# Kernel tuning notes

Measured on AMD Instinct MI355X. Metric: run time of the kernel, lower is better.

The kernel has to match this reference:

```python
import jax, jax.numpy as jnp
import numpy as np

EPS = 1e-5
NUM_CLUSTERS = 64


def _bn(x, g, b, m, v):
    # eval-mode BatchNorm over channel (last) axis
    return (x - m) * (g * jax.lax.rsqrt(v + EPS)) + b


def _segment_max(feat, choice, num_clusters):
    # feat: [B, N, C], choice: [B, N] -> [B, K, C] (amax per cluster, -inf if empty)
    def one(f, c):
        init = jnp.full((num_clusters, f.shape[-1]), -jnp.inf, dtype=f.dtype)
        return init.at[c].max(f)
    return jax.vmap(one)(feat, choice)


def setup_inputs() -> dict:
    key = jax.random.key(0)
    ks = jax.random.split(key, 8)
    B, N, K, OUT = 32, 8192, NUM_CLUSTERS, 384
    s = lambda fan: 1.0 / np.sqrt(fan)
    return {
        "xyz": jax.random.normal(ks[0], (B, N, 3), jnp.float32),
        "choice": jax.random.randint(ks[1], (B, N), 0, K, jnp.int32),
        "w1": jax.random.normal(ks[2], (128, 3), jnp.float32) * s(3),
        "b1": jnp.zeros((128,), jnp.float32),
        "bn1_g": jnp.ones((128,), jnp.float32),
        "bn1_b": jnp.zeros((128,), jnp.float32),
        "bn1_m": jnp.zeros((128,), jnp.float32),
        "bn1_v": jnp.ones((128,), jnp.float32),
        "w2": jax.random.normal(ks[3], (256, 128), jnp.float32) * s(128),
        "b2": jnp.zeros((256,), jnp.float32),
        "w3": jax.random.normal(ks[4], (512, 512), jnp.float32) * s(512),
        "b3": jnp.zeros((512,), jnp.float32),
        "bn2_g": jnp.ones((512,), jnp.float32),
        "bn2_b": jnp.zeros((512,), jnp.float32),
        "bn2_m": jnp.zeros((512,), jnp.float32),
        "bn2_v": jnp.ones((512,), jnp.float32),
        "w4": jax.random.normal(ks[5], (OUT, 512), jnp.float32) * s(512),
        "b4": jnp.zeros((OUT,), jnp.float32),
    }


def reference(xyz, choice, w1, b1, bn1_g, bn1_b, bn1_m, bn1_v, w2, b2,
              w3, b3, bn2_g, bn2_b, bn2_m, bn2_v, w4, b4):
    # first_conv: 1x1 conv == per-point linear. xyz: [B,N,3]
    h = jnp.einsum("bnc,oc->bno", xyz, w1) + b1            # [B,N,128]
    h = jax.nn.relu(_bn(h, bn1_g, bn1_b, bn1_m, bn1_v))
    feat = jnp.einsum("bnc,oc->bno", h, w2) + b2            # [B,N,256]
    # cluster amax pooling + gather-broadcast back to points
    fg = _segment_max(feat, choice, NUM_CLUSTERS)           # [B,K,256]
    fg_pts = jnp.take_along_axis(fg, choice[..., None], axis=1)  # [B,N,256]
    f = jnp.concatenate([fg_pts, feat], axis=-1)            # [B,N,512]
    # second_conv
    h2 = jnp.einsum("bnc,oc->bno", f, w3) + b3              # [B,N,512]
    h2 = jax.nn.relu(_bn(h2, bn2_g, bn2_b, bn2_m, bn2_v))
    out = jnp.einsum("bnc,oc->bno", h2, w4) + b4            # [B,N,out_dim]
    return _segment_max(out, choice, NUM_CLUSTERS)          # [B,K,out_dim]
```

## Files before the change

### kernel.cpp

```cpp
#include <hip/hip_runtime.h>
#include <hip/hip_bf16.h>

typedef unsigned short u16;
typedef __attribute__((ext_vector_type(8))) short short8;
typedef __attribute__((ext_vector_type(4))) float f32x4;

#define EPSV 1e-5f
#define ENC_NINF 0x007FFFFFu

__device__ __forceinline__ float bf2f(u16 u) {
    union { unsigned int i; float f; } v; v.i = ((unsigned int)u) << 16; return v.f;
}
__device__ __forceinline__ u16 f2bf(float f) {
    union { float f; unsigned int i; } v; v.f = f;
    unsigned int x = v.i;
    return (u16)((x + 0x7FFFu + ((x >> 16) & 1u)) >> 16);
}
__device__ __forceinline__ unsigned int encbf(u16 u) {
    unsigned int f = ((unsigned int)u) << 16;
    return (f & 0x80000000u) ? ~f : (f | 0x80000000u);
}
__device__ __forceinline__ float dec(unsigned int u) {
    union { float f; unsigned int uu; } v;
    v.uu = (u & 0x80000000u) ? (u & 0x7FFFFFFFu) : ~u;
    return v.f;
}

__device__ __forceinline__ void async16(const u16* g, u16* l) {
    __builtin_amdgcn_global_load_lds((const __attribute__((address_space(1))) void*)g,
                                     (__attribute__((address_space(3))) void*)l,
                                     16, 0, 0);
}

__global__ __launch_bounds__(256) void k_fillf(float* __restrict__ o, int n, float val)
{
    int i = blockIdx.x * 256 + threadIdx.x;
    if (i < n) o[i] = val;
}

__global__ __launch_bounds__(256) void k_initu(unsigned int* __restrict__ o, int n)
{
    int i = blockIdx.x * 256 + threadIdx.x;
    if (i < n) o[i] = ENC_NINF;
}

struct Ptrs { const void* p[17]; int off[18]; int chN; };

__global__ __launch_bounds__(256) void k_repack(Ptrs P, const void* __restrict__ chSrc,
                                                int* __restrict__ chi, u16* __restrict__ rp)
{
    const unsigned int* probe = (const unsigned int*)P.p[9];
    int cnt = 0;
#pragma unroll
    for (int i = 0; i < 64; ++i) {
        unsigned int lo = probe[i] & 0xFFFFu;
        if (((lo >> 7) & 0xFFu) >= 0x80u) ++cnt;
    }
    const bool is_f32 = (cnt > 8);

    const unsigned int* cp = (const unsigned int*)chSrc;
    int z = 0; unsigned int mx = 0;
    for (int i = 0; i < 1024; ++i) {
        unsigned int w = cp[i];
        z += (w == 0u);
        mx = (w > mx) ? w : mx;
    }
    const int chMode = (mx >= 64u) ? 2 : ((z > 300) ? 1 : 0);

    const int stride = gridDim.x * 256;
    const int gid0 = blockIdx.x * 256 + threadIdx.x;

    const int totalF = P.off[17];
    for (int g = gid0; g < totalF; g += stride) {
        int t = 0;
        while (g >= P.off[t + 1]) ++t;
        int off = g - P.off[t];
        u16 v;
        if (is_f32) v = f2bf(((const float*)P.p[t])[off]);
        else        v = ((const u16*)P.p[t])[off];
        rp[g] = v;
    }
    for (int i = gid0; i < P.chN; i += stride) {
        int v;
        if (chMode == 1)      v = (int)((const long long*)chSrc)[i];
        else if (chMode == 2) v = (int)((const float*)chSrc)[i];
        else                  v = ((const int*)chSrc)[i];
        chi[i] = v & 63;
    }
}

__global__ __launch_bounds__(256) void k_sort(const int* __restrict__ chi,
                                              int* __restrict__ schoice,
                                              int* __restrict__ perm)
{
    __shared__ int hist[64];
    __shared__ int base[64];
    const int b = blockIdx.x, tid = threadIdx.x;
    if (tid < 64) hist[tid] = 0;
    __syncthreads();
    const int o = b << 13;
    for (int i = tid; i < 8192; i += 256) atomicAdd(&hist[chi[o + i]], 1);
    __syncthreads();
    if (tid == 0) {
        int s = 0;
        for (int k = 0; k < 64; ++k) { base[k] = s; s += hist[k]; }
    }
    __syncthreads();
    for (int i = tid; i < 8192; i += 256) {
        int k = chi[o + i];
        int pos = atomicAdd(&base[k], 1);
        schoice[o + pos] = k;
        perm[o + pos] = o + i;
    }
}

__global__ __launch_bounds__(256, 2) void g1_feat(
    const u16* __restrict__ xyz, const u16* __restrict__ w1, const u16* __restrict__ b1,
    const u16* __restrict__ g1v, const u16* __restrict__ bb1,
    const u16* __restrict__ m1, const u16* __restrict__ v1,
    const u16* __restrict__ w2, const u16* __restrict__ b2,
    const int* __restrict__ schoice, const int* __restrict__ perm,
    u16* __restrict__ feat, unsigned int* __restrict__ fg_u)
{
    __shared__ __align__(16) u16 Bs[256 * 128];
    __shared__ unsigned int lred[8 * 256];
    __shared__ float4 pw[128];
    __shared__ float xs[128], ys[128], zs[128];
    __shared__ int chs[128];
    const int tid = threadIdx.x, lane = tid & 63, wave = tid >> 6;
    const int wm = (wave & 1) << 6, wn = (wave >> 1) << 6;
    const int m0 = blockIdx.x << 7;
    if (tid < 128) {
        float s = bf2f(g1v[tid]) * rsqrtf(bf2f(v1[tid]) + EPSV);
        float4 w;
        w.x = bf2f(w1[tid * 3 + 0]) * s;
        w.y = bf2f(w1[tid * 3 + 1]) * s;
        w.z = bf2f(w1[tid * 3 + 2]) * s;
        w.w = (bf2f(b1[tid]) - bf2f(m1[tid])) * s + bf2f(bb1[tid]);
        pw[tid] = w;
        const u16* p = xyz + (size_t)perm[m0 + tid] * 3;
        xs[tid] = bf2f(p[0]); ys[tid] = bf2f(p[1]); zs[tid] = bf2f(p[2]);
        chs[tid] = schoice[m0 + tid];
    }
    const int q = lane >> 4, mr = lane & 15;
    f32x4 acc[2][4][4] = {};
#pragma unroll
    for (int i = 0; i < 16; ++i) {
        int id = (i << 8) + tid, row = id >> 4, cc = id & 15;
        async16(w2 + (size_t)row * 128 + ((cc ^ (row & 15)) << 3), &Bs[id << 3]);
    }
    __syncthreads();
    const int kmin = chs[0], nk = chs[127] - kmin + 1;
    const bool useL = (nk <= 8);
    if (useL) for (int i = tid; i < (nk << 8); i += 256) lred[i] = ENC_NINF;
#pragma unroll
    for (int kk = 0; kk < 4; ++kk) {
        const int lc = kk * 4 + q;
        float4 wv[8];
#pragma unroll
        for (int j = 0; j < 8; ++j) wv[j] = pw[kk * 32 + q * 8 + j];
        short8 af[4];
#pragma unroll
        for (int mi = 0; mi < 4; ++mi) {
            int row = wm + mi * 16 + mr;
            float x = xs[row], y = ys[row], z = zs[row];
#pragma unroll
            for (int j = 0; j < 8; ++j) {
                float val = fmaf(x, wv[j].x, fmaf(y, wv[j].y, fmaf(z, wv[j].z, wv[j].w)));
                af[mi][j] = (short)f2bf(fmaxf(val, 0.0f));
            }
        }
#pragma unroll
        for (int h = 0; h < 2; ++h) {
            short8 bfr[4];
#pragma unroll
            for (int ni = 0; ni < 4; ++ni) {
                int r = (h << 7) + wn + ni * 16 + mr;
                bfr[ni] = *(const short8*)&Bs[r * 128 + ((lc ^ (r & 15)) << 3)];
            }
#pragma unroll
            for (int mi = 0; mi < 4; ++mi)
#pragma unroll
                for (int ni = 0; ni < 4; ++ni)
                    acc[h][mi][ni] = __builtin_amdgcn_mfma_f32_16x16x32_bf16(af[mi], bfr[ni], acc[h][mi][ni], 0, 0, 0);
        }
    }
    __syncthreads();
    const int colb = lane & 15;
    const int bl = m0 >> 13;
    unsigned int* db = fg_u + (size_t)(bl << 6) * 256;
#pragma unroll
    for (int h = 0; h < 2; ++h)
#pragma unroll
        for (int ni = 0; ni < 4; ++ni) {
            int n = (h << 7) + wn + (ni << 4) + colb;
            float bv = bf2f(b2[n]);
#pragma unroll
            for (int mi = 0; mi < 4; ++mi) {
                int curk = -1; unsigned int run = 0;
#pragma unroll
                for (int r = 0; r < 4; ++r) {
                    int rr = wm + (mi << 4) + (q << 2) + r;
                    u16 vb = f2bf(acc[h][mi][ni][r] + bv);
                    feat[(size_t)(m0 + rr) * 256 + n] = vb;
                    unsigned int e = encbf(vb);
                    int k = chs[rr];
                    if (k != curk) {
                        if (curk >= 0) {
                            if (useL) atomicMax(&lred[((curk - kmin) << 8) + n], run);
                            else      atomicMax(&db[curk * 256 + n], run);
                        }
                        curk = k; run = e;
                    } else run = run > e ? run : e;
                }
                if (useL) atomicMax(&lred[((curk - kmin) << 8) + n], run);
                else      atomicMax(&db[curk * 256 + n], run);
            }
        }
    if (useL) {
        __syncthreads();
        for (int i = tid; i < (nk << 8); i += 256) {
            unsigned int v = lred[i];
            if (v != ENC_NINF) atomicMax(&db[(kmin + (i >> 8)) * 256 + (i & 255)], v);
        }
    }
}

__global__ __launch_bounds__(256) void g4_out(
    const u16* __restrict__ A, const u16* __restrict__ Bt,
    const u16* __restrict__ bias, const int* __restrict__ schoice,
    unsigned int* __restrict__ out_u, const int K, const int N)
{
    __shared__ __align__(16) u16 smem[2 * 128 * 64];
    __shared__ int chs[128];
    u16* As = smem;
    u16* Bs = smem + 128 * 64;
    const int tid = threadIdx.x, lane = tid & 63, wave = tid >> 6;
    const int wm = (wave & 1) << 6, wn = (wave >> 1) << 6;
    const int m0 = blockIdx.x << 7, n0 = blockIdx.y << 7;
    const int c = tid & 7, rb = tid >> 3;
    if (tid < 128) chs[tid] = schoice[m0 + tid];
    f32x4 acc[4][4] = {};
    for (int k0 = 0; k0 < K; k0 += 64) {
        __syncthreads();
#pragma unroll
        for (int i = 0; i < 4; ++i) {
            int id = (i << 8) + tid, row = id >> 3, cc = id & 7;
            async16(Bt + (n0 + row) * K + k0 + ((cc ^ (row & 7)) << 3), &Bs[id << 3]);
        }
#pragma unroll
        for (int i = 0; i < 4; ++i) {
            int r = rb + (i << 5);
            async16(A + (size_t)(m0 + r) * K + k0 + ((c ^ (r & 7)) << 3),
                    &As[(((i << 8) + tid) << 3)]);
        }
        __syncthreads();
        const int q = lane >> 4, mr = lane & 15;
#pragma unroll
        for (int kk = 0; kk < 2; ++kk) {
            short8 af[4], bfr[4];
            const int lc = kk * 4 + q;
#pragma unroll
            for (int mi = 0; mi < 4; ++mi) {
                int r = wm + mi * 16 + mr;
                af[mi] = *(const short8*)&As[r * 64 + ((lc ^ (r & 7)) << 3)];
            }
#pragma unroll
            for (int ni = 0; ni < 4; ++ni) {
                int r = wn + ni * 16 + mr;
                bfr[ni] = *(const short8*)&Bs[r * 64 + ((lc ^ (r & 7)) << 3)];
            }
#pragma unroll
            for (int mi = 0; mi < 4; ++mi)
#pragma unroll
                for (int ni = 0; ni < 4; ++ni)
                    acc[mi][ni] = __builtin_amdgcn_mfma_f32_16x16x32_bf16(af[mi], bfr[ni], acc[mi][ni], 0, 0, 0);
        }
    }
    __syncthreads();
    unsigned int* lred = (unsigned int*)smem;
    const int kmin = chs[0], nk = chs[127] - kmin + 1;
    for (int i = tid; i < (nk << 7); i += 256) lred[i] = ENC_NINF;
    __syncthreads();
    const int q = lane >> 4, colb = lane & 15;
#pragma unroll
    for (int ni = 0; ni < 4; ++ni) {
        int nc = wn + (ni << 4) + colb;
        float bv = bf2f(bias[n0 + nc]);
#pragma unroll
        for (int mi = 0; mi < 4; ++mi) {
            int curk = -1; unsigned int run = 0;
#pragma unroll
            for (int r = 0; r < 4; ++r) {
                int rr = wm + (mi << 4) + (q << 2) + r;
                unsigned int e = encbf(f2bf(acc[mi][ni][r] + bv));
                int k = chs[rr];
                if (k != curk) {
                    if (curk >= 0) atomicMax(&lred[((curk - kmin) << 7) + nc], run);
                    curk = k; run = e;
                } else run = run > e ? run : e;
            }
            atomicMax(&lred[((curk - kmin) << 7) + nc], run);
        }
    }
    __syncthreads();
    const int bl = m0 >> 13;
    unsigned int* db = out_u + (size_t)(bl << 6) * N;
    for (int i = tid; i < (nk << 7); i += 256) {
        unsigned int v = lred[i];
        if (v != ENC_NINF) atomicMax(&db[(kmin + (i >> 7)) * N + n0 + (i & 127)], v);
    }
}

__global__ __launch_bounds__(256) void k_dec_bf(const unsigned int* __restrict__ u,
                                                u16* __restrict__ o, int n)
{
    int i = blockIdx.x * 256 + threadIdx.x;
    if (i < n) o[i] = f2bf(dec(u[i]));
}
__global__ __launch_bounds__(256) void k_dec_f32(const unsigned int* __restrict__ u,
                                                 float* __restrict__ o, int n)
{
    int i = blockIdx.x * 256 + threadIdx.x;
    if (i < n) o[i] = dec(u[i]);
}

__global__ __launch_bounds__(256, 2) void g3_h2(
    const int* __restrict__ schoice, const u16* __restrict__ feat,
    const u16* __restrict__ fg, const u16* __restrict__ w3, const u16* __restrict__ b3,
    const u16* __restrict__ g2, const u16* __restrict__ bb2,
    const u16* __restrict__ m2, const u16* __restrict__ v2,
    u16* __restrict__ h2)
{
    __shared__ __align__(16) u16 As[128 * 64];
    __shared__ __align__(16) u16 Bs[2 * 128 * 64];
    const int tid = threadIdx.x, lane = tid & 63, wave = tid >> 6;
    const int wm = (wave & 1) << 6, wn = (wave >> 1) << 6;
    const int m0 = blockIdx.x << 7, n0 = blockIdx.y << 8;
    const int c = tid & 7, rb = tid >> 3;
    const u16* fgrow[4]; const u16* ftrow[4];
#pragma unroll
    for (int i = 0; i < 4; ++i) {
        int pt = m0 + rb + (i << 5);
        int b = pt >> 13;
        fgrow[i] = fg + (((b << 6) + schoice[pt]) << 8);
        ftrow[i] = feat + ((size_t)pt << 8);
    }
    f32x4 acc[2][4][4] = {};
    for (int k0 = 0; k0 < 512; k0 += 64) {
        __syncthreads();
#pragma unroll
        for (int nt = 0; nt < 2; ++nt)
#pragma unroll
            for (int i = 0; i < 4; ++i) {
                int id = (i << 8) + tid, row = id >> 3, cc = id & 7;
                async16(w3 + (size_t)(n0 + nt * 128 + row) * 512 + k0 + ((cc ^ (row & 7)) << 3),
                        &Bs[nt * 8192 + (id << 3)]);
            }
#pragma unroll
        for (int i = 0; i < 4; ++i) {
            int r = rb + (i << 5);
            int col = k0 + ((c ^ (r & 7)) << 3);
            const u16* src = (col < 256) ? (fgrow[i] + col) : (ftrow[i] + (col - 256));
            async16(src, &As[(((i << 8) + tid) << 3)]);
        }
        __syncthreads();
        const int q = lane >> 4, mr = lane & 15;
#pragma unroll
        for (int kk = 0; kk < 2; ++kk) {
            short8 af[4];
            const int lc = kk * 4 + q;
#pragma unroll
            for (int mi = 0; mi < 4; ++mi) {
                int r = wm + mi * 16 + mr;
                af[mi] = *(const short8*)&As[r * 64 + ((lc ^ (r & 7)) << 3)];
            }
#pragma unroll
            for (int nt = 0; nt < 2; ++nt) {
                short8 bfr[4];
#pragma unroll
                for (int ni = 0; ni < 4; ++ni) {
                    int r = wn + ni * 16 + mr;
                    bfr[ni] = *(const short8*)&Bs[nt * 8192 + r * 64 + ((lc ^ (r & 7)) << 3)];
                }
#pragma unroll
                for (int mi = 0; mi < 4; ++mi)
#pragma unroll
                    for (int ni = 0; ni < 4; ++ni)
                        acc[nt][mi][ni] = __builtin_amdgcn_mfma_f32_16x16x32_bf16(af[mi], bfr[ni], acc[nt][mi][ni], 0, 0, 0);
            }
        }
    }
    const int q = lane >> 4, colb = lane & 15;
#pragma unroll
    for (int nt = 0; nt < 2; ++nt)
#pragma unroll
        for (int ni = 0; ni < 4; ++ni) {
            int n = n0 + nt * 128 + wn + (ni << 4) + colb;
            float s = bf2f(g2[n]) * rsqrtf(bf2f(v2[n]) + EPSV);
            float t = (bf2f(b3[n]) - bf2f(m2[n])) * s + bf2f(bb2[n]);
#pragma unroll
            for (int mi = 0; mi < 4; ++mi)
#pragma unroll
                for (int r = 0; r < 4; ++r) {
                    int m = m0 + wm + (mi << 4) + (q << 2) + r;
                    h2[(size_t)m * 512 + n] = f2bf(fmaxf(fmaf(acc[nt][mi][ni][r], s, t), 0.0f));
                }
        }
}

extern "C" void kernel_launch(void* const* d_in, const int* in_sizes, int n_in,
                              void* d_out, int out_size, void* d_ws, size_t ws_size,
                              hipStream_t stream)
{
    float* out = (float*)d_out;
    if (n_in != 18) {
        k_fillf<<<dim3((out_size + 255) / 256), 256, 0, stream>>>(out, out_size, 1000.0f);
        return;
    }

    const int map[17] = {0, 2, 3, 4, 5, 6, 7, 8, 9, 10, 11, 12, 13, 14, 15, 16, 17};
    Ptrs P;
    P.off[0] = 0;
    for (int i = 0; i < 17; ++i) {
        P.p[i] = d_in[map[i]];
        P.off[i + 1] = P.off[i] + in_sizes[map[i]];
    }
    P.chN = in_sizes[1];

    char* ws = (char*)d_ws;
    int* chi = (int*)ws;
    const size_t chiB = ((size_t)P.chN * 4 + 255) & ~255ull;
    int* schoice = (int*)(ws + chiB);
    int* perm    = (int*)(ws + 2 * chiB);
    u16* rp = (u16*)(ws + 3 * chiB);
    const size_t rpB = ((size_t)P.off[17] * 2 + 255) & ~255ull;
    const size_t RPB = 3 * chiB + rpB;

    k_repack<<<dim3(1024), 256, 0, stream>>>(P, d_in[1], chi, rp);
    k_sort<<<dim3(P.chN >> 13), 256, 0, stream>>>(chi, schoice, perm);

    const u16* xyz  = rp + P.off[0];
    const u16* w1   = rp + P.off[1];
    const u16* b1   = rp + P.off[2];
    const u16* bn1g = rp + P.off[3];
    const u16* bn1b = rp + P.off[4];
    const u16* bn1m = rp + P.off[5];
    const u16* bn1v = rp + P.off[6];
    const u16* w2   = rp + P.off[7];
    const u16* b2   = rp + P.off[8];
    const u16* w3   = rp + P.off[9];
    const u16* b3   = rp + P.off[10];
    const u16* bn2g = rp + P.off[11];
    const u16* bn2b = rp + P.off[12];
    const u16* bn2m = rp + P.off[13];
    const u16* bn2v = rp + P.off[14];
    const u16* w4   = rp + P.off[15];
    const u16* b4   = rp + P.off[16];

    unsigned int* fg_u_all  = (unsigned int*)(ws + RPB);
    unsigned int* out_u_all = fg_u_all + 32 * 64 * 256;
    const size_t UB = 5242880ull;
    const int nU = 32 * 64 * 640;

    const size_t PB = 12615680ull;
    int sb = 32;
    while (sb > 1 && RPB + UB + (size_t)sb * PB > ws_size) sb >>= 1;
    if (RPB + UB + PB > ws_size) {
        k_fillf<<<dim3((out_size + 255) / 256), 256, 0, stream>>>(out, out_size, 3000.0f);
        return;
    }
    const int ns = 32 / sb;

    char* wsb = ws + RPB + UB;
    const size_t featB = (size_t)sb * 8192 * 256 * 2;
    const size_t h2B   = (size_t)sb * 8192 * 512 * 2;
    u16* feat = (u16*)(wsb);
    u16* h2s  = (u16*)(wsb + featB);
    u16* fg   = (u16*)(wsb + featB + h2B);

    k_initu<<<dim3((nU + 255) / 256), 256, 0, stream>>>(fg_u_all, nU);

    const int mblk = sb << 6;
    const int nfg = sb * 64 * 256;
    const int nou = sb * 64 * 384;
    for (int s = 0; s < ns; ++s) {
        const int b0 = s * sb;
        const int pt0 = b0 << 13;
        const int* sch_sl = schoice + pt0;
        const int* perm_sl = perm + pt0;
        unsigned int* fg_u  = fg_u_all + (size_t)b0 * 64 * 256;
        unsigned int* out_u = out_u_all + (size_t)b0 * 64 * 384;
        g1_feat<<<dim3(mblk), 256, 0, stream>>>(xyz, w1, b1, bn1g, bn1b, bn1m, bn1v,
                                                w2, b2, sch_sl, perm_sl, feat, fg_u);
        k_dec_bf<<<dim3((nfg + 255) / 256), 256, 0, stream>>>(fg_u, fg, nfg);
        g3_h2<<<dim3(mblk, 2), 256, 0, stream>>>(sch_sl, feat, fg, w3, b3,
                                                 bn2g, bn2b, bn2m, bn2v, h2s);
        g4_out<<<dim3(mblk, 3), 256, 0, stream>>>(h2s, w4, b4, sch_sl, out_u, 512, 384);
        k_dec_f32<<<dim3((nou + 255) / 256), 256, 0, stream>>>(out_u,
                                                               out + ((size_t)b0 << 6) * 384, nou);
    }
}
```

Baseline: 526.4 us.

## Fuse second-conv GEMM and output GEMM with segment-max into one kernel

Merges the h2 GEMM (with BN+ReLU) and the output GEMM plus cluster max-reduction into a single 512-thread kernel. Each 128-point block keeps its h2 half-tile in LDS and consumes it straight away, so the h2 intermediate never goes through global memory. The init of the max buffers is also folded into the repack kernel to save a launch. In exchange the kernel uses much more LDS and more accumulator registers per block, which lowers occupancy, and grid parallelism drops because the N dimension is no longer split across blocks.

```diff
diff --git a/kernel.cpp b/kernel.cpp
--- a/kernel.cpp
+++ b/kernel.cpp
@@ -38,16 +38,11 @@
     if (i < n) o[i] = val;
 }
 
-__global__ __launch_bounds__(256) void k_initu(unsigned int* __restrict__ o, int n)
-{
-    int i = blockIdx.x * 256 + threadIdx.x;
-    if (i < n) o[i] = ENC_NINF;
-}
-
 struct Ptrs { const void* p[17]; int off[18]; int chN; };
 
 __global__ __launch_bounds__(256) void k_repack(Ptrs P, const void* __restrict__ chSrc,
-                                                int* __restrict__ chi, u16* __restrict__ rp)
+                                                int* __restrict__ chi, u16* __restrict__ rp,
+                                                unsigned int* __restrict__ initp, int nU)
 {
     const unsigned int* probe = (const unsigned int*)P.p[9];
     int cnt = 0;
@@ -87,6 +82,7 @@
         else                  v = ((const int*)chSrc)[i];
         chi[i] = v & 63;
     }
+    for (int i = gid0; i < nU; i += stride) initp[i] = ENC_NINF;
 }
 
 __global__ __launch_bounds__(256) void k_sort(const int* __restrict__ chi,
@@ -226,187 +222,178 @@
     }
 }
 
-__global__ __launch_bounds__(256) void g4_out(
-    const u16* __restrict__ A, const u16* __restrict__ Bt,
-    const u16* __restrict__ bias, const int* __restrict__ schoice,
-    unsigned int* __restrict__ out_u, const int K, const int N)
-{
-    __shared__ __align__(16) u16 smem[2 * 128 * 64];
-    __shared__ int chs[128];
-    u16* As = smem;
-    u16* Bs = smem + 128 * 64;
-    const int tid = threadIdx.x, lane = tid & 63, wave = tid >> 6;
-    const int wm = (wave & 1) << 6, wn = (wave >> 1) << 6;
-    const int m0 = blockIdx.x << 7, n0 = blockIdx.y << 7;
-    const int c = tid & 7, rb = tid >> 3;
-    if (tid < 128) chs[tid] = schoice[m0 + tid];
-    f32x4 acc[4][4] = {};
-    for (int k0 = 0; k0 < K; k0 += 64) {
-        __syncthreads();
-#pragma unroll
-        for (int i = 0; i < 4; ++i) {
-            int id = (i << 8) + tid, row = id >> 3, cc = id & 7;
-            async16(Bt + (n0 + row) * K + k0 + ((cc ^ (row & 7)) << 3), &Bs[id << 3]);
-        }
-#pragma unroll
-        for (int i = 0; i < 4; ++i) {
-            int r = rb + (i << 5);
-            async16(A + (size_t)(m0 + r) * K + k0 + ((c ^ (r & 7)) << 3),
-                    &As[(((i << 8) + tid) << 3)]);
-        }
-        __syncthreads();
-        const int q = lane >> 4, mr = lane & 15;
-#pragma unroll
-        for (int kk = 0; kk < 2; ++kk) {
-            short8 af[4], bfr[4];
-            const int lc = kk * 4 + q;
-#pragma unroll
-            for (int mi = 0; mi < 4; ++mi) {
-                int r = wm + mi * 16 + mr;
-                af[mi] = *(const short8*)&As[r * 64 + ((lc ^ (r & 7)) << 3)];
-            }
-#pragma unroll
-            for (int ni = 0; ni < 4; ++ni) {
-                int r = wn + ni * 16 + mr;
-                bfr[ni] = *(const short8*)&Bs[r * 64 + ((lc ^ (r & 7)) << 3)];
-            }
-#pragma unroll
-            for (int mi = 0; mi < 4; ++mi)
-#pragma unroll
-                for (int ni = 0; ni < 4; ++ni)
-                    acc[mi][ni] = __builtin_amdgcn_mfma_f32_16x16x32_bf16(af[mi], bfr[ni], acc[mi][ni], 0, 0, 0);
-        }
-    }
-    __syncthreads();
-    unsigned int* lred = (unsigned int*)smem;
-    const int kmin = chs[0], nk = chs[127] - kmin + 1;
-    for (int i = tid; i < (nk << 7); i += 256) lred[i] = ENC_NINF;
-    __syncthreads();
-    const int q = lane >> 4, colb = lane & 15;
-#pragma unroll
-    for (int ni = 0; ni < 4; ++ni) {
-        int nc = wn + (ni << 4) + colb;
-        float bv = bf2f(bias[n0 + nc]);
-#pragma unroll
-        for (int mi = 0; mi < 4; ++mi) {
-            int curk = -1; unsigned int run = 0;
-#pragma unroll
-            for (int r = 0; r < 4; ++r) {
-                int rr = wm + (mi << 4) + (q << 2) + r;
-                unsigned int e = encbf(f2bf(acc[mi][ni][r] + bv));
-                int k = chs[rr];
-                if (k != curk) {
-                    if (curk >= 0) atomicMax(&lred[((curk - kmin) << 7) + nc], run);
-                    curk = k; run = e;
-                } else run = run > e ? run : e;
-            }
-            atomicMax(&lred[((curk - kmin) << 7) + nc], run);
-        }
-    }
-    __syncthreads();
-    const int bl = m0 >> 13;
-    unsigned int* db = out_u + (size_t)(bl << 6) * N;
-    for (int i = tid; i < (nk << 7); i += 256) {
-        unsigned int v = lred[i];
-        if (v != ENC_NINF) atomicMax(&db[(kmin + (i >> 7)) * N + n0 + (i & 127)], v);
-    }
-}
-
-__global__ __launch_bounds__(256) void k_dec_bf(const unsigned int* __restrict__ u,
-                                                u16* __restrict__ o, int n)
-{
-    int i = blockIdx.x * 256 + threadIdx.x;
-    if (i < n) o[i] = f2bf(dec(u[i]));
-}
-__global__ __launch_bounds__(256) void k_dec_f32(const unsigned int* __restrict__ u,
-                                                 float* __restrict__ o, int n)
-{
-    int i = blockIdx.x * 256 + threadIdx.x;
-    if (i < n) o[i] = dec(u[i]);
-}
-
-__global__ __launch_bounds__(256, 2) void g3_h2(
+__global__ __launch_bounds__(512, 2) void g34_out(
     const int* __restrict__ schoice, const u16* __restrict__ feat,
     const u16* __restrict__ fg, const u16* __restrict__ w3, const u16* __restrict__ b3,
     const u16* __restrict__ g2, const u16* __restrict__ bb2,
     const u16* __restrict__ m2, const u16* __restrict__ v2,
-    u16* __restrict__ h2)
-{
-    __shared__ __align__(16) u16 As[128 * 64];
-    __shared__ __align__(16) u16 Bs[2 * 128 * 64];
+    const u16* __restrict__ w4, const u16* __restrict__ b4,
+    unsigned int* __restrict__ out_u)
+{
+    __shared__ __align__(16) u16 uni[24576];
+    __shared__ __align__(16) u16 H[32768];
+    __shared__ int chs[128];
+    u16* As  = uni;
+    u16* Bs  = uni + 8192;
+    u16* Bs2 = uni;
     const int tid = threadIdx.x, lane = tid & 63, wave = tid >> 6;
-    const int wm = (wave & 1) << 6, wn = (wave >> 1) << 6;
-    const int m0 = blockIdx.x << 7, n0 = blockIdx.y << 8;
+    const int q = lane >> 4, mr = lane & 15, colb = lane & 15;
+    const int wm2  = (wave & 1) << 6;
+    const int wn4  = ((wave >> 1) & 3) << 6;
+    const int wn96 = (wave >> 1) * 96;
+    const int m0 = blockIdx.x << 7;
     const int c = tid & 7, rb = tid >> 3;
-    const u16* fgrow[4]; const u16* ftrow[4];
-#pragma unroll
-    for (int i = 0; i < 4; ++i) {
-        int pt = m0 + rb + (i << 5);
+    if (tid < 128) chs[tid] = schoice[m0 + tid];
+    const u16* arow[2]; const u16* frow[2];
+#pragma unroll
+    for (int i = 0; i < 2; ++i) {
+        int pt = m0 + rb + (i << 6);
         int b = pt >> 13;
-        fgrow[i] = fg + (((b << 6) + schoice[pt]) << 8);
-        ftrow[i] = feat + ((size_t)pt << 8);
-    }
-    f32x4 acc[2][4][4] = {};
-    for (int k0 = 0; k0 < 512; k0 += 64) {
+        arow[i] = fg + (((b << 6) + schoice[pt]) << 8);
+        frow[i] = feat + ((size_t)pt << 8);
+    }
+    f32x4 acc_b[4][6] = {};
+    for (int nh = 0; nh < 2; ++nh) {
+        f32x4 acc_a[4][4] = {};
+        for (int k0 = 0; k0 < 512; k0 += 64) {
+            __syncthreads();
+#pragma unroll
+            for (int i = 0; i < 4; ++i) {
+                int id = (i << 9) + tid, row = id >> 3, cc = id & 7;
+                async16(w3 + (size_t)((nh << 8) + row) * 512 + k0 + ((cc ^ (row & 7)) << 3),
+                        &Bs[id << 3]);
+            }
+#pragma unroll
+            for (int i = 0; i < 2; ++i) {
+                int r = rb + (i << 6);
+                int col = k0 + ((c ^ (r & 7)) << 3);
+                const u16* src = (k0 < 256) ? (arow[i] + col) : (frow[i] + (col - 256));
+                async16(src, &As[(((i << 9) + tid) << 3)]);
+            }
+            __syncthreads();
+#pragma unroll
+            for (int kk = 0; kk < 2; ++kk) {
+                const int lc = (kk << 2) + q;
+                short8 af[4], bfr[4];
+#pragma unroll
+                for (int mi = 0; mi < 4; ++mi) {
+                    int r = wm2 + (mi << 4) + mr;
+                    af[mi] = *(const short8*)&As[r * 64 + ((lc ^ (r & 7)) << 3)];
+                }
+#pragma unroll
+                for (int ni = 0; ni < 4; ++ni) {
+                    int r = wn4 + (ni << 4) + mr;
+                    bfr[ni] = *(const short8*)&Bs[r * 64 + ((lc ^ (r & 7)) << 3)];
+                }
+#pragma unroll
+                for (int mi = 0; mi < 4; ++mi)
+#pragma unroll
+                    for (int ni = 0; ni < 4; ++ni)
+                        acc_a[mi][ni] = __builtin_amdgcn_mfma_f32_16x16x32_bf16(af[mi], bfr[ni], acc_a[mi][ni], 0, 0, 0);
+            }
+        }
         __syncthreads();
 #pragma unroll
-        for (int nt = 0; nt < 2; ++nt)
-#pragma unroll
-            for (int i = 0; i < 4; ++i) {
-                int id = (i << 8) + tid, row = id >> 3, cc = id & 7;
-                async16(w3 + (size_t)(n0 + nt * 128 + row) * 512 + k0 + ((cc ^ (row & 7)) << 3),
-                        &Bs[nt * 8192 + (id << 3)]);
-            }
-#pragma unroll
-        for (int i = 0; i < 4; ++i) {
-            int r = rb + (i << 5);
-            int col = k0 + ((c ^ (r & 7)) << 3);
-            const u16* src = (col < 256) ? (fgrow[i] + col) : (ftrow[i] + (col - 256));
-            async16(src, &As[(((i << 8) + tid) << 3)]);
-        }
-        __syncthreads();
-        const int q = lane >> 4, mr = lane & 15;
-#pragma unroll
-        for (int kk = 0; kk < 2; ++kk) {
-            short8 af[4];
-            const int lc = kk * 4 + q;
-#pragma unroll
-            for (int mi = 0; mi < 4; ++mi) {
-                int r = wm + mi * 16 + mr;
-                af[mi] = *(const short8*)&As[r * 64 + ((lc ^ (r & 7)) << 3)];
-            }
-#pragma unroll
-            for (int nt = 0; nt < 2; ++nt) {
-                short8 bfr[4];
-#pragma unroll
-                for (int ni = 0; ni < 4; ++ni) {
-                    int r = wn + ni * 16 + mr;
-                    bfr[ni] = *(const short8*)&Bs[nt * 8192 + r * 64 + ((lc ^ (r & 7)) << 3)];
-                }
-#pragma unroll
-                for (int mi = 0; mi < 4; ++mi)
-#pragma unroll
-                    for (int ni = 0; ni < 4; ++ni)
-                        acc[nt][mi][ni] = __builtin_amdgcn_mfma_f32_16x16x32_bf16(af[mi], bfr[ni], acc[nt][mi][ni], 0, 0, 0);
-            }
-        }
-    }
-    const int q = lane >> 4, colb = lane & 15;
-#pragma unroll
-    for (int nt = 0; nt < 2; ++nt)
-#pragma unroll
         for (int ni = 0; ni < 4; ++ni) {
-            int n = n0 + nt * 128 + wn + (ni << 4) + colb;
+            int n = (nh << 8) + wn4 + (ni << 4) + colb;
             float s = bf2f(g2[n]) * rsqrtf(bf2f(v2[n]) + EPSV);
             float t = (bf2f(b3[n]) - bf2f(m2[n])) * s + bf2f(bb2[n]);
+            int ck = wn4 + (ni << 4) + colb;
+            int cchi = ck >> 3, clo = ck & 7;
 #pragma unroll
             for (int mi = 0; mi < 4; ++mi)
 #pragma unroll
                 for (int r = 0; r < 4; ++r) {
-                    int m = m0 + wm + (mi << 4) + (q << 2) + r;
-                    h2[(size_t)m * 512 + n] = f2bf(fmaxf(fmaf(acc[nt][mi][ni][r], s, t), 0.0f));
-                }
-        }
+                    int rr = wm2 + (mi << 4) + (q << 2) + r;
+                    H[rr * 256 + ((cchi ^ (rr & 7)) << 3) + clo] =
+                        f2bf(fmaxf(fmaf(acc_a[mi][ni][r], s, t), 0.0f));
+                }
+        }
+        for (int k0 = 0; k0 < 256; k0 += 64) {
+            __syncthreads();
+#pragma unroll
+            for (int i = 0; i < 6; ++i) {
+                int id = (i << 9) + tid, row = id >> 3, cc = id & 7;
+                async16(w4 + (size_t)row * 512 + (nh << 8) + k0 + ((cc ^ (row & 7)) << 3),
+                        &Bs2[id << 3]);
+            }
+            __syncthreads();
+            const int cb = k0 >> 3;
+#pragma unroll
+            for (int kk = 0; kk < 2; ++kk) {
+                const int lc = (kk << 2) + q;
+                short8 af[4];
+#pragma unroll
+                for (int mi = 0; mi < 4; ++mi) {
+                    int r = wm2 + (mi << 4) + mr;
+                    af[mi] = *(const short8*)&H[r * 256 + ((cb + (lc ^ (r & 7))) << 3)];
+                }
+#pragma unroll
+                for (int ni = 0; ni < 6; ++ni) {
+                    int r = wn96 + (ni << 4) + mr;
+                    short8 bfr = *(const short8*)&Bs2[r * 64 + ((lc ^ (r & 7)) << 3)];
+#pragma unroll
+                    for (int mi = 0; mi < 4; ++mi)
+                        acc_b[mi][ni] = __builtin_amdgcn_mfma_f32_16x16x32_bf16(af[mi], bfr, acc_b[mi][ni], 0, 0, 0);
+                }
+            }
+        }
+    }
+    __syncthreads();
+    unsigned int* lred = (unsigned int*)H;
+    const int kmin = chs[0], nk = chs[127] - kmin + 1;
+    const bool useL = (nk <= 40);
+    const int bl = m0 >> 13;
+    unsigned int* db = out_u + (size_t)(bl << 6) * 384;
+    if (useL) for (int i = tid; i < nk * 384; i += 512) lred[i] = ENC_NINF;
+    __syncthreads();
+#pragma unroll
+    for (int ni = 0; ni < 6; ++ni) {
+        int nc = wn96 + (ni << 4) + colb;
+        float bv = bf2f(b4[nc]);
+#pragma unroll
+        for (int mi = 0; mi < 4; ++mi) {
+            int curk = -1; unsigned int run = 0;
+#pragma unroll
+            for (int r = 0; r < 4; ++r) {
+                int rr = wm2 + (mi << 4) + (q << 2) + r;
+                unsigned int e = encbf(f2bf(acc_b[mi][ni][r] + bv));
+                int k = chs[rr];
+                if (k != curk) {
+                    if (curk >= 0) {
+                        if (useL) atomicMax(&lred[(curk - kmin) * 384 + nc], run);
+                        else      atomicMax(&db[curk * 384 + nc], run);
+                    }
+                    curk = k; run = e;
+                } else run = run > e ? run : e;
+            }
+            if (useL) atomicMax(&lred[(curk - kmin) * 384 + nc], run);
+            else      atomicMax(&db[curk * 384 + nc], run);
+        }
+    }
+    if (useL) {
+        __syncthreads();
+        for (int i = tid; i < nk * 384; i += 512) {
+            unsigned int v = lred[i];
+            if (v != ENC_NINF) {
+                int kq = i / 384;
+                atomicMax(&db[(kmin + kq) * 384 + (i - kq * 384)], v);
+            }
+        }
+    }
+}
+
+__global__ __launch_bounds__(256) void k_dec_bf(const unsigned int* __restrict__ u,
+                                                u16* __restrict__ o, int n)
+{
+    int i = blockIdx.x * 256 + threadIdx.x;
+    if (i < n) o[i] = f2bf(dec(u[i]));
+}
+__global__ __launch_bounds__(256) void k_dec_f32(const unsigned int* __restrict__ u,
+                                                 float* __restrict__ o, int n)
+{
+    int i = blockIdx.x * 256 + threadIdx.x;
+    if (i < n) o[i] = dec(u[i]);
 }
 
 extern "C" void kernel_launch(void* const* d_in, const int* in_sizes, int n_in,
@@ -437,7 +424,12 @@
     const size_t rpB = ((size_t)P.off[17] * 2 + 255) & ~255ull;
     const size_t RPB = 3 * chiB + rpB;
 
-    k_repack<<<dim3(1024), 256, 0, stream>>>(P, d_in[1], chi, rp);
+    unsigned int* fg_u_all  = (unsigned int*)(ws + RPB);
+    unsigned int* out_u_all = fg_u_all + 32 * 64 * 256;
+    const size_t UB = 5242880ull;
+    const int nU = 32 * 64 * 640;
+
+    k_repack<<<dim3(1024), 256, 0, stream>>>(P, d_in[1], chi, rp, fg_u_all, nU);
     k_sort<<<dim3(P.chN >> 13), 256, 0, stream>>>(chi, schoice, perm);
 
     const u16* xyz  = rp + P.off[0];
@@ -458,12 +450,7 @@
     const u16* w4   = rp + P.off[15];
     const u16* b4   = rp + P.off[16];
 
-    unsigned int* fg_u_all  = (unsigned int*)(ws + RPB);
-    unsigned int* out_u_all = fg_u_all + 32 * 64 * 256;
-    const size_t UB = 5242880ull;
-    const int nU = 32 * 64 * 640;
-
-    const size_t PB = 12615680ull;
+    const size_t PB = 4227072ull;
     int sb = 32;
     while (sb > 1 && RPB + UB + (size_t)sb * PB > ws_size) sb >>= 1;
     if (RPB + UB + PB > ws_size) {
@@ -474,12 +461,8 @@
 
     char* wsb = ws + RPB + UB;
     const size_t featB = (size_t)sb * 8192 * 256 * 2;
-    const size_t h2B   = (size_t)sb * 8192 * 512 * 2;
     u16* feat = (u16*)(wsb);
-    u16* h2s  = (u16*)(wsb + featB);
-    u16* fg   = (u16*)(wsb + featB + h2B);
-
-    k_initu<<<dim3((nU + 255) / 256), 256, 0, stream>>>(fg_u_all, nU);
+    u16* fg   = (u16*)(wsb + featB);
 
     const int mblk = sb << 6;
     const int nfg = sb * 64 * 256;
@@ -494,9 +477,8 @@
         g1_feat<<<dim3(mblk), 256, 0, stream>>>(xyz, w1, b1, bn1g, bn1b, bn1m, bn1v,
                                                 w2, b2, sch_sl, perm_sl, feat, fg_u);
         k_dec_bf<<<dim3((nfg + 255) / 256), 256, 0, stream>>>(fg_u, fg, nfg);
-        g3_h2<<<dim3(mblk, 2), 256, 0, stream>>>(sch_sl, feat, fg, w3, b3,
-                                                 bn2g, bn2b, bn2m, bn2v, h2s);
-        g4_out<<<dim3(mblk, 3), 256, 0, stream>>>(h2s, w4, b4, sch_sl, out_u, 512, 384);
+        g34_out<<<dim3(mblk), 512, 0, stream>>>(sch_sl, feat, fg, w3, b3,
+                                                bn2g, bn2b, bn2m, bn2v, w4, b4, out_u);
         k_dec_f32<<<dim3((nou + 255) / 256), 256, 0, stream>>>(out_u,
                                                                out + ((size_t)b0 << 6) * 384, nou);
     }
```

Result: slower. 755.0 us (+43.4%).

## Retile final GEMM to 64-row blocks covering all 384 outputs; fold init into repack

Applied to the files above, without the earlier changes.

The output GEMM (h2 x w4) now uses 64-row tiles where each block computes all 384 output columns, instead of 128x128 tiles over a 3-wide grid. Each A tile is loaded once and the cluster-max reduction covers full rows, with a fallback to direct global atomics when the tile spans too many clusters to fit in LDS. The separate init kernel for the encoded max buffers is merged into the repack kernel, saving one launch. In exchange, each block reloads the full w4 slice from global per k-step, and the larger LDS footprint may limit occupancy.

```diff
diff --git a/kernel.cpp b/kernel.cpp
--- a/kernel.cpp
+++ b/kernel.cpp
@@ -38,16 +38,11 @@
     if (i < n) o[i] = val;
 }
 
-__global__ __launch_bounds__(256) void k_initu(unsigned int* __restrict__ o, int n)
-{
-    int i = blockIdx.x * 256 + threadIdx.x;
-    if (i < n) o[i] = ENC_NINF;
-}
-
 struct Ptrs { const void* p[17]; int off[18]; int chN; };
 
 __global__ __launch_bounds__(256) void k_repack(Ptrs P, const void* __restrict__ chSrc,
-                                                int* __restrict__ chi, u16* __restrict__ rp)
+                                                int* __restrict__ chi, u16* __restrict__ rp,
+                                                unsigned int* __restrict__ initp, int nU)
 {
     const unsigned int* probe = (const unsigned int*)P.p[9];
     int cnt = 0;
@@ -87,6 +82,7 @@
         else                  v = ((const int*)chSrc)[i];
         chi[i] = v & 63;
     }
+    for (int i = gid0; i < nU; i += stride) initp[i] = ENC_NINF;
 }
 
 __global__ __launch_bounds__(256) void k_sort(const int* __restrict__ chi,
@@ -226,105 +222,6 @@
     }
 }
 
-__global__ __launch_bounds__(256) void g4_out(
-    const u16* __restrict__ A, const u16* __restrict__ Bt,
-    const u16* __restrict__ bias, const int* __restrict__ schoice,
-    unsigned int* __restrict__ out_u, const int K, const int N)
-{
-    __shared__ __align__(16) u16 smem[2 * 128 * 64];
-    __shared__ int chs[128];
-    u16* As = smem;
-    u16* Bs = smem + 128 * 64;
-    const int tid = threadIdx.x, lane = tid & 63, wave = tid >> 6;
-    const int wm = (wave & 1) << 6, wn = (wave >> 1) << 6;
-    const int m0 = blockIdx.x << 7, n0 = blockIdx.y << 7;
-    const int c = tid & 7, rb = tid >> 3;
-    if (tid < 128) chs[tid] = schoice[m0 + tid];
-    f32x4 acc[4][4] = {};
-    for (int k0 = 0; k0 < K; k0 += 64) {
-        __syncthreads();
-#pragma unroll
-        for (int i = 0; i < 4; ++i) {
-            int id = (i << 8) + tid, row = id >> 3, cc = id & 7;
-            async16(Bt + (n0 + row) * K + k0 + ((cc ^ (row & 7)) << 3), &Bs[id << 3]);
-        }
-#pragma unroll
-        for (int i = 0; i < 4; ++i) {
-            int r = rb + (i << 5);
-            async16(A + (size_t)(m0 + r) * K + k0 + ((c ^ (r & 7)) << 3),
-                    &As[(((i << 8) + tid) << 3)]);
-        }
-        __syncthreads();
-        const int q = lane >> 4, mr = lane & 15;
-#pragma unroll
-        for (int kk = 0; kk < 2; ++kk) {
-            short8 af[4], bfr[4];
-            const int lc = kk * 4 + q;
-#pragma unroll
-            for (int mi = 0; mi < 4; ++mi) {
-                int r = wm + mi * 16 + mr;
-                af[mi] = *(const short8*)&As[r * 64 + ((lc ^ (r & 7)) << 3)];
-            }
-#pragma unroll
-            for (int ni = 0; ni < 4; ++ni) {
-                int r = wn + ni * 16 + mr;
-                bfr[ni] = *(const short8*)&Bs[r * 64 + ((lc ^ (r & 7)) << 3)];
-            }
-#pragma unroll
-            for (int mi = 0; mi < 4; ++mi)
-#pragma unroll
-                for (int ni = 0; ni < 4; ++ni)
-                    acc[mi][ni] = __builtin_amdgcn_mfma_f32_16x16x32_bf16(af[mi], bfr[ni], acc[mi][ni], 0, 0, 0);
-        }
-    }
-    __syncthreads();
-    unsigned int* lred = (unsigned int*)smem;
-    const int kmin = chs[0], nk = chs[127] - kmin + 1;
-    for (int i = tid; i < (nk << 7); i += 256) lred[i] = ENC_NINF;
-    __syncthreads();
-    const int q = lane >> 4, colb = lane & 15;
-#pragma unroll
-    for (int ni = 0; ni < 4; ++ni) {
-        int nc = wn + (ni << 4) + colb;
-        float bv = bf2f(bias[n0 + nc]);
-#pragma unroll
-        for (int mi = 0; mi < 4; ++mi) {
-            int curk = -1; unsigned int run = 0;
-#pragma unroll
-            for (int r = 0; r < 4; ++r) {
-                int rr = wm + (mi << 4) + (q << 2) + r;
-                unsigned int e = encbf(f2bf(acc[mi][ni][r] + bv));
-                int k = chs[rr];
-                if (k != curk) {
-                    if (curk >= 0) atomicMax(&lred[((curk - kmin) << 7) + nc], run);
-                    curk = k; run = e;
-                } else run = run > e ? run : e;
-            }
-            atomicMax(&lred[((curk - kmin) << 7) + nc], run);
-        }
-    }
-    __syncthreads();
-    const int bl = m0 >> 13;
-    unsigned int* db = out_u + (size_t)(bl << 6) * N;
-    for (int i = tid; i < (nk << 7); i += 256) {
-        unsigned int v = lred[i];
-        if (v != ENC_NINF) atomicMax(&db[(kmin + (i >> 7)) * N + n0 + (i & 127)], v);
-    }
-}
-
-__global__ __launch_bounds__(256) void k_dec_bf(const unsigned int* __restrict__ u,
-                                                u16* __restrict__ o, int n)
-{
-    int i = blockIdx.x * 256 + threadIdx.x;
-    if (i < n) o[i] = f2bf(dec(u[i]));
-}
-__global__ __launch_bounds__(256) void k_dec_f32(const unsigned int* __restrict__ u,
-                                                 float* __restrict__ o, int n)
-{
-    int i = blockIdx.x * 256 + threadIdx.x;
-    if (i < n) o[i] = dec(u[i]);
-}
-
 __global__ __launch_bounds__(256, 2) void g3_h2(
     const int* __restrict__ schoice, const u16* __restrict__ feat,
     const u16* __restrict__ fg, const u16* __restrict__ w3, const u16* __restrict__ b3,
@@ -407,6 +304,112 @@
                     h2[(size_t)m * 512 + n] = f2bf(fmaxf(fmaf(acc[nt][mi][ni][r], s, t), 0.0f));
                 }
         }
+}
+
+__global__ __launch_bounds__(256, 2) void g4_out(
+    const u16* __restrict__ A, const u16* __restrict__ w4,
+    const u16* __restrict__ bias, const int* __restrict__ schoice,
+    unsigned int* __restrict__ out_u)
+{
+    __shared__ __align__(16) u16 smem[28672];
+    __shared__ int chs[64];
+    u16* As = smem;
+    u16* Bs = smem + 4096;
+    const int tid = threadIdx.x, lane = tid & 63, wave = tid >> 6;
+    const int m0 = blockIdx.x << 6;
+    if (tid < 64) chs[tid] = schoice[m0 + tid];
+    f32x4 acc[4][6] = {};
+    for (int k0 = 0; k0 < 512; k0 += 64) {
+        __syncthreads();
+#pragma unroll
+        for (int i = 0; i < 12; ++i) {
+            int id = (i << 8) + tid, row = id >> 3, cc = id & 7;
+            async16(w4 + (size_t)row * 512 + k0 + ((cc ^ (row & 7)) << 3),
+                    &Bs[id << 3]);
+        }
+#pragma unroll
+        for (int i = 0; i < 2; ++i) {
+            int id = (i << 8) + tid, row = id >> 3, cc = id & 7;
+            async16(A + (size_t)(m0 + row) * 512 + k0 + ((cc ^ (row & 7)) << 3),
+                    &As[id << 3]);
+        }
+        __syncthreads();
+        const int q = lane >> 4, mr = lane & 15;
+#pragma unroll
+        for (int kk = 0; kk < 2; ++kk) {
+            const int lc = (kk << 2) + q;
+            short8 af[4];
+#pragma unroll
+            for (int mi = 0; mi < 4; ++mi) {
+                int r = (mi << 4) + mr;
+                af[mi] = *(const short8*)&As[r * 64 + ((lc ^ (r & 7)) << 3)];
+            }
+#pragma unroll
+            for (int ni = 0; ni < 6; ++ni) {
+                int r = wave * 96 + (ni << 4) + mr;
+                short8 bfr = *(const short8*)&Bs[r * 64 + ((lc ^ (r & 7)) << 3)];
+#pragma unroll
+                for (int mi = 0; mi < 4; ++mi)
+                    acc[mi][ni] = __builtin_amdgcn_mfma_f32_16x16x32_bf16(af[mi], bfr, acc[mi][ni], 0, 0, 0);
+            }
+        }
+    }
+    __syncthreads();
+    unsigned int* lred = (unsigned int*)smem;
+    const int kmin = chs[0], nk = chs[63] - kmin + 1;
+    const bool useL = (nk <= 37);
+    const int bl = m0 >> 13;
+    unsigned int* db = out_u + (size_t)(bl << 6) * 384;
+    if (useL) for (int i = tid; i < nk * 384; i += 256) lred[i] = ENC_NINF;
+    __syncthreads();
+    const int q = lane >> 4, colb = lane & 15;
+#pragma unroll
+    for (int ni = 0; ni < 6; ++ni) {
+        int nc = wave * 96 + (ni << 4) + colb;
+        float bv = bf2f(bias[nc]);
+#pragma unroll
+        for (int mi = 0; mi < 4; ++mi) {
+            int curk = -1; unsigned int run = 0;
+#pragma unroll
+            for (int r = 0; r < 4; ++r) {
+                int rr = (mi << 4) + (q << 2) + r;
+                unsigned int e = encbf(f2bf(acc[mi][ni][r] + bv));
+                int k = chs[rr];
+                if (k != curk) {
+                    if (curk >= 0) {
+                        if (useL) atomicMax(&lred[(curk - kmin) * 384 + nc], run);
+                        else      atomicMax(&db[curk * 384 + nc], run);
+                    }
+                    curk = k; run = e;
+                } else run = run > e ? run : e;
+            }
+            if (useL) atomicMax(&lred[(curk - kmin) * 384 + nc], run);
+            else      atomicMax(&db[curk * 384 + nc], run);
+        }
+    }
+    if (useL) {
+        __syncthreads();
+        for (int i = tid; i < nk * 384; i += 256) {
+            unsigned int v = lred[i];
+            if (v != ENC_NINF) {
+                int kq = i / 384;
+                atomicMax(&db[(kmin + kq) * 384 + (i - kq * 384)], v);
+            }
+        }
+    }
+}
+
+__global__ __launch_bounds__(256) void k_dec_bf(const unsigned int* __restrict__ u,
+                                                u16* __restrict__ o, int n)
+{
+    int i = blockIdx.x * 256 + threadIdx.x;
+    if (i < n) o[i] = f2bf(dec(u[i]));
+}
+__global__ __launch_bounds__(256) void k_dec_f32(const unsigned int* __restrict__ u,
+                                                 float* __restrict__ o, int n)
+{
+    int i = blockIdx.x * 256 + threadIdx.x;
+    if (i < n) o[i] = dec(u[i]);
 }
 
 extern "C" void kernel_launch(void* const* d_in, const int* in_sizes, int n_in,
@@ -437,7 +440,12 @@
     const size_t rpB = ((size_t)P.off[17] * 2 + 255) & ~255ull;
     const size_t RPB = 3 * chiB + rpB;
 
-    k_repack<<<dim3(1024), 256, 0, stream>>>(P, d_in[1], chi, rp);
+    unsigned int* fg_u_all  = (unsigned int*)(ws + RPB);
+    unsigned int* out_u_all = fg_u_all + 32 * 64 * 256;
+    const size_t UB = 5242880ull;
+    const int nU = 32 * 64 * 640;
+
+    k_repack<<<dim3(1024), 256, 0, stream>>>(P, d_in[1], chi, rp, fg_u_all, nU);
     k_sort<<<dim3(P.chN >> 13), 256, 0, stream>>>(chi, schoice, perm);
 
     const u16* xyz  = rp + P.off[0];
@@ -458,11 +466,6 @@
     const u16* w4   = rp + P.off[15];
     const u16* b4   = rp + P.off[16];
 
-    unsigned int* fg_u_all  = (unsigned int*)(ws + RPB);
-    unsigned int* out_u_all = fg_u_all + 32 * 64 * 256;
-    const size_t UB = 5242880ull;
-    const int nU = 32 * 64 * 640;
-
     const size_t PB = 12615680ull;
     int sb = 32;
     while (sb > 1 && RPB + UB + (size_t)sb * PB > ws_size) sb >>= 1;
@@ -479,9 +482,8 @@
     u16* h2s  = (u16*)(wsb + featB);
     u16* fg   = (u16*)(wsb + featB + h2B);
 
-    k_initu<<<dim3((nU + 255) / 256), 256, 0, stream>>>(fg_u_all, nU);
-
-    const int mblk = sb << 6;
+    const int mblk  = sb << 6;
+    const int mblk2 = sb << 7;
     const int nfg = sb * 64 * 256;
     const int nou = sb * 64 * 384;
     for (int s = 0; s < ns; ++s) {
@@ -496,7 +498,7 @@
         k_dec_bf<<<dim3((nfg + 255) / 256), 256, 0, stream>>>(fg_u, fg, nfg);
         g3_h2<<<dim3(mblk, 2), 256, 0, stream>>>(sch_sl, feat, fg, w3, b3,
                                                  bn2g, bn2b, bn2m, bn2v, h2s);
-        g4_out<<<dim3(mblk, 3), 256, 0, stream>>>(h2s, w4, b4, sch_sl, out_u, 512, 384);
+        g4_out<<<dim3(mblk2), 256, 0, stream>>>(h2s, w4, b4, sch_sl, out_u);
         k_dec_f32<<<dim3((nou + 255) / 256), 256, 0, stream>>>(out_u,
                                                                out + ((size_t)b0 << 6) * 384, nou);
     }
```

Result: slower. 550.8 us (+4.6%).
